# Kernel optimization log

Hardware: AMD Instinct MI355X
Metric: run time of the kernel (lower is better)

The kernel has to match this reference:

```python
import jax, jax.numpy as jnp
import numpy as np

EMBED_DIM = 1024
NUM_HEADS = 16
D_K = EMBED_DIM // NUM_HEADS


def setup_inputs() -> dict:
    key = jax.random.key(0)
    kx, kq, kk, kv, ko = jax.random.split(key, 5)
    scale = 1.0 / np.sqrt(EMBED_DIM)
    x = jax.random.normal(kx, (4, 2048, EMBED_DIM), dtype=jnp.float32)
    # Linear(embed_dim, embed_dim, bias=False) weights, stored [out, in] like torch
    Wq = jax.random.uniform(kq, (EMBED_DIM, EMBED_DIM), jnp.float32, -scale, scale)
    Wk = jax.random.uniform(kk, (EMBED_DIM, EMBED_DIM), jnp.float32, -scale, scale)
    Wv = jax.random.uniform(kv, (EMBED_DIM, EMBED_DIM), jnp.float32, -scale, scale)
    Wo = jax.random.uniform(ko, (EMBED_DIM, EMBED_DIM), jnp.float32, -scale, scale)
    return {"x": x, "Wq": Wq, "Wk": Wk, "Wv": Wv, "Wo": Wo}


def reference(x, Wq, Wk, Wv, Wo):
    b, s, _ = x.shape
    # torch Linear: y = x @ W.T
    def proj(W):
        y = jnp.einsum('bse,fe->bsf', x, W)
        return y.reshape(b, s, NUM_HEADS, D_K).transpose(0, 2, 1, 3)  # [b,h,s,d]
    q, k, v = proj(Wq), proj(Wk), proj(Wv)
    scores = jnp.einsum('bhqd,bhkd->bhqk', q, k) / jnp.sqrt(jnp.float32(D_K))
    attn = jax.nn.softmax(scores, axis=-1)  # dropout is identity in eval
    out = jnp.einsum('bhqk,bhkd->bhqd', attn, v)
    out = out.transpose(0, 2, 1, 3).reshape(b, s, EMBED_DIM)
    return jnp.einsum('bsf,ef->bse', out, Wo)
```

## Files before the change

### kernel.cpp

```cpp
#include <hip/hip_runtime.h>
#include <hip/hip_bf16.h>

typedef unsigned short u16;
typedef unsigned int   u32;
typedef __attribute__((ext_vector_type(8))) __bf16 bf16x8;
typedef __attribute__((ext_vector_type(2))) __bf16 bf16x2;
typedef __attribute__((ext_vector_type(8))) u16    ushort8v;
typedef __attribute__((ext_vector_type(2))) float  f32x2;
typedef __attribute__((ext_vector_type(4))) float  floatx4;

#define EMBED 1024
#define SEQ   2048
#define BATCH 4
#define NH    16
#define DKH   64
#define BHN   (BATCH*NH)
#define ZSTRIDE ((size_t)BHN*SEQ*DKH)

__device__ __forceinline__ u16 f2bf(float f){
  union { float f; unsigned u; } v; v.f = f;
  unsigned r = (v.u + 0x7FFFu + ((v.u >> 16) & 1u)) >> 16;
  return (u16)r;
}
__device__ __forceinline__ u32 pk2(float a, float b){
  f32x2 v = {a, b};
  return __builtin_bit_cast(u32, __builtin_convertvector(v, bf16x2));
}

__device__ __forceinline__ bf16x8 ld_frag(const u16* p){
  return __builtin_bit_cast(bf16x8, *(const ushort8v*)p);
}

__device__ __forceinline__ floatx4 mfma16(bf16x8 a, bf16x8 b, floatx4 c){
  return __builtin_amdgcn_mfma_f32_16x16x32_bf16(a, b, c, 0, 0, 0);
}

__device__ __forceinline__ void gl_lds16(const u16* g, u16* l){
  __builtin_amdgcn_global_load_lds((const __attribute__((address_space(1))) void*)g,
                                   (__attribute__((address_space(3))) void*)l,
                                   16, 0, 0);
}

#define CFENCE asm volatile("" ::: "memory")

__global__ __launch_bounds__(256) void cvt_all(const float* __restrict__ x,
    const float* __restrict__ wq, const float* __restrict__ wk,
    const float* __restrict__ wv, const float* __restrict__ wo,
    u16* __restrict__ Xb, u16* __restrict__ Wqb, u16* __restrict__ Wkb,
    u16* __restrict__ Wvb, u16* __restrict__ Wob){
  int b = blockIdx.x;
  const float* src; u16* dst; int i;
  if (b < 8192){ src = x; dst = Xb; i = b*256 + threadIdx.x; }
  else {
    int k = (b - 8192) >> 10, r = (b - 8192) & 1023;
    src = (k==0) ? wq : (k==1) ? wk : (k==2) ? wv : wo;
    dst = (k==0) ? Wqb : (k==1) ? Wkb : (k==2) ? Wvb : Wob;
    i = r*256 + threadIdx.x;
  }
  float4 v = ((const float4*)src)[i];
  ushort4 o;
  o.x = f2bf(v.x); o.y = f2bf(v.y); o.z = f2bf(v.z); o.w = f2bf(v.w);
  ((ushort4*)dst)[i] = o;
}

#define QSCALE 0.1803368801111204f
__global__ __launch_bounds__(256, 2) void gemm_qkv(const u16* __restrict__ X,
    const u16* __restrict__ Wq, const u16* __restrict__ Wk, const u16* __restrict__ Wv,
    u16* __restrict__ QKV){
  __shared__ __attribute__((aligned(16))) u16 As[2*128*32];
  __shared__ __attribute__((aligned(16))) u16 Bs[3][2*128*32];

  const int tid = threadIdx.x, lane = tid & 63, w = tid >> 6;
  const int lm = lane & 15, quad = lane >> 4;
  const int wm = (w & 1) * 64, wn = (w >> 1) * 64;
  const int m0 = blockIdx.x * 128, n0 = blockIdx.y * 128;
  const int row0 = tid >> 2, kc = tid & 3;

  const u16* A0 = X  + (size_t)(m0 + row0)*EMBED + kc*8;
  const u16* B0[3] = {
    Wq + (size_t)(n0 + row0)*EMBED + kc*8,
    Wk + (size_t)(n0 + row0)*EMBED + kc*8,
    Wv + (size_t)(n0 + row0)*EMBED + kc*8 };

  floatx4 acc[3][4][4];
  #pragma unroll
  for (int z = 0; z < 3; ++z)
    #pragma unroll
    for (int mi = 0; mi < 4; ++mi)
      #pragma unroll
      for (int ni = 0; ni < 4; ++ni)
        acc[z][mi][ni] = (floatx4){0.f, 0.f, 0.f, 0.f};

  gl_lds16(A0,            As + tid*8);
  gl_lds16(A0 + 64*EMBED, As + (256 + tid)*8);
  #pragma unroll
  for (int z = 0; z < 3; ++z){
    gl_lds16(B0[z],            Bs[z] + tid*8);
    gl_lds16(B0[z] + 64*EMBED, Bs[z] + (256 + tid)*8);
  }

  for (int kt = 0; kt < EMBED/32; ++kt){
    const int cur = kt & 1;
    __builtin_amdgcn_s_barrier();
    CFENCE;
    if (kt + 1 < EMBED/32){
      const int k0 = (kt + 1) * 32;
      gl_lds16(A0 + k0,            As + (cur^1)*4096 + tid*8);
      gl_lds16(A0 + 64*EMBED + k0, As + (cur^1)*4096 + (256 + tid)*8);
      #pragma unroll
      for (int z = 0; z < 3; ++z){
        gl_lds16(B0[z] + k0,            Bs[z] + (cur^1)*4096 + tid*8);
        gl_lds16(B0[z] + 64*EMBED + k0, Bs[z] + (cur^1)*4096 + (256 + tid)*8);
      }
      asm volatile("s_waitcnt vmcnt(8)" ::: "memory");
    } else {
      asm volatile("s_waitcnt vmcnt(0)" ::: "memory");
    }
    __builtin_amdgcn_s_barrier();
    CFENCE;
    const u16* Ac = As + cur*4096;
    bf16x8 af[4];
    #pragma unroll
    for (int mi = 0; mi < 4; ++mi)
      af[mi] = ld_frag(&Ac[(wm + mi*16 + lm)*32 + quad*8]);
    #pragma unroll
    for (int z = 0; z < 3; ++z){
      const u16* Bc = Bs[z] + cur*4096;
      bf16x8 bfz[4];
      #pragma unroll
      for (int ni = 0; ni < 4; ++ni)
        bfz[ni] = ld_frag(&Bc[(wn + ni*16 + lm)*32 + quad*8]);
      #pragma unroll
      for (int mi = 0; mi < 4; ++mi)
        #pragma unroll
        for (int ni = 0; ni < 4; ++ni)
          acc[z][mi][ni] = mfma16(af[mi], bfz[ni], acc[z][mi][ni]);
    }
  }

  #pragma unroll
  for (int z = 0; z < 2; ++z){
    const float scale = (z == 0) ? QSCALE : 1.0f;
    u16* outz = QKV + (size_t)z * ZSTRIDE;
    #pragma unroll
    for (int mi = 0; mi < 4; ++mi)
      #pragma unroll
      for (int ni = 0; ni < 4; ++ni)
        #pragma unroll
        for (int r = 0; r < 4; ++r){
          int m = m0 + wm + mi*16 + quad*4 + r;
          int n = n0 + wn + ni*16 + lm;
          int b = m >> 11, s = m & 2047, h = n >> 6, d = n & 63;
          outz[(((size_t)(b*NH + h))*SEQ + s)*DKH + d] = f2bf(acc[z][mi][ni][r] * scale);
        }
  }
  {
    u16* outz = QKV + (size_t)2 * ZSTRIDE;
    #pragma unroll
    for (int mi = 0; mi < 4; ++mi)
      #pragma unroll
      for (int ni = 0; ni < 4; ++ni){
        int mbase = m0 + wm + mi*16 + quad*4;
        int n = n0 + wn + ni*16 + lm;
        int b = mbase >> 11, sb = mbase & 2047;
        int h = n >> 6, d = n & 63;
        u16* dst = outz + (((size_t)(b*NH + h))*DKH + d)*SEQ + sb;
        uint2 pv;
        pv.x = pk2(acc[2][mi][ni][0], acc[2][mi][ni][1]);
        pv.y = pk2(acc[2][mi][ni][2], acc[2][mi][ni][3]);
        *reinterpret_cast<uint2*>(dst) = pv;
      }
  }
}

__global__ __launch_bounds__(256) void gemm_out(const u16* __restrict__ A,
    const u16* __restrict__ W, float* __restrict__ C){
  __shared__ __attribute__((aligned(16))) u16 As[2*128*64];
  __shared__ __attribute__((aligned(16))) u16 Bs[2*128*64];
  const int tid = threadIdx.x, lane = tid & 63, w = tid >> 6;
  const int lm = lane & 15, quad = lane >> 4;
  const int wm = (w & 1) * 64, wn = (w >> 1) * 64;
  const int m0 = blockIdx.x * 128, n0 = blockIdx.y * 128;

  const int srow = tid >> 3;
  const int ssw  = ((tid & 7) ^ (srow & 7)) * 8;
  const u16* Ab = A + (size_t)(m0 + srow)*EMBED + ssw;
  const u16* Bb = W + (size_t)(n0 + srow)*EMBED + ssw;

  floatx4 acc[4][4];
  #pragma unroll
  for (int mi = 0; mi < 4; ++mi)
    #pragma unroll
    for (int ni = 0; ni < 4; ++ni)
      acc[mi][ni] = (floatx4){0.f, 0.f, 0.f, 0.f};

  #pragma unroll
  for (int j = 0; j < 4; ++j){
    gl_lds16(Ab + (size_t)j*32*EMBED, As + (j*256 + tid)*8);
    gl_lds16(Bb + (size_t)j*32*EMBED, Bs + (j*256 + tid)*8);
  }

  for (int kt = 0; kt < EMBED/64; ++kt){
    const int cur = kt & 1;
    __builtin_amdgcn_s_barrier();
    CFENCE;
    if (kt + 1 < EMBED/64){
      const int k0 = (kt + 1) * 64;
      #pragma unroll
      for (int j = 0; j < 4; ++j){
        gl_lds16(Ab + (size_t)j*32*EMBED + k0, As + (cur^1)*8192 + (j*256 + tid)*8);
        gl_lds16(Bb + (size_t)j*32*EMBED + k0, Bs + (cur^1)*8192 + (j*256 + tid)*8);
      }
      asm volatile("s_waitcnt vmcnt(8)" ::: "memory");
    } else {
      asm volatile("s_waitcnt vmcnt(0)" ::: "memory");
    }
    __builtin_amdgcn_s_barrier();
    CFENCE;
    const u16* Ac = As + cur*8192;
    const u16* Bc = Bs + cur*8192;
    #pragma unroll
    for (int kh = 0; kh < 2; ++kh){
      const int us = ((kh*4 + quad) ^ (lm & 7)) * 8;
      bf16x8 af[4], bf[4];
      #pragma unroll
      for (int mi = 0; mi < 4; ++mi)
        af[mi] = ld_frag(&Ac[(wm + mi*16 + lm)*64 + us]);
      #pragma unroll
      for (int ni = 0; ni < 4; ++ni)
        bf[ni] = ld_frag(&Bc[(wn + ni*16 + lm)*64 + us]);
      #pragma unroll
      for (int mi = 0; mi < 4; ++mi)
        #pragma unroll
        for (int ni = 0; ni < 4; ++ni)
          acc[mi][ni] = mfma16(af[mi], bf[ni], acc[mi][ni]);
    }
  }

  #pragma unroll
  for (int mi = 0; mi < 4; ++mi)
    #pragma unroll
    for (int ni = 0; ni < 4; ++ni)
      #pragma unroll
      for (int r = 0; r < 4; ++r){
        int m = m0 + wm + mi*16 + quad*4 + r;
        int n = n0 + wn + ni*16 + lm;
        C[(size_t)m*EMBED + n] = acc[mi][ni][r];
      }
}

#define KSS 520
__global__ __launch_bounds__(256, 2) void attn_kernel(const u16* __restrict__ QKV,
                                                      u16* __restrict__ Out){
  __shared__ __attribute__((aligned(16))) u16 Ks[2][8*KSS];
  __shared__ __attribute__((aligned(16))) u16 Vs[2][64*64];

  const int tid = threadIdx.x, lane = tid & 63, w = tid >> 6;
  const int lm = lane & 15, quad = lane >> 4;
  const int bh = blockIdx.x;
  const int q0 = blockIdx.y * 256;
  const u16* Qh = QKV + (size_t)bh * SEQ * DKH;
  const u16* Kh = QKV + ZSTRIDE + (size_t)bh * SEQ * DKH;
  const u16* Vh = QKV + 2*ZSTRIDE + (size_t)bh * DKH * SEQ;

  const int sK = tid & 63, cK = tid >> 6;
  const int dV = tid >> 3, gV = tid & 7;
  const size_t vsrc0 = (size_t)dV * SEQ + ((gV ^ (dV & 7)) * 8);
  const size_t vsrc1 = vsrc0 + (size_t)32 * SEQ;

  bf16x8 qf[4][2];
  #pragma unroll
  for (int qt = 0; qt < 4; ++qt)
    #pragma unroll
    for (int st = 0; st < 2; ++st)
      qf[qt][st] = ld_frag(Qh + (size_t)(q0 + w*64 + qt*16 + lm)*DKH + st*32 + quad*8);

  const uint4 ONESW = {0x3F803F80u, 0x3F803F80u, 0x3F803F80u, 0x3F803F80u};
  const bf16x8 ones8 = __builtin_bit_cast(bf16x8, ONESW);

  floatx4 o[4][4], lac[4];
  #pragma unroll
  for (int qt = 0; qt < 4; ++qt){
    lac[qt] = (floatx4){0.f, 0.f, 0.f, 0.f};
    #pragma unroll
    for (int dt = 0; dt < 4; ++dt) o[qt][dt] = (floatx4){0.f, 0.f, 0.f, 0.f};
  }

  gl_lds16(Kh + (size_t)sK*DKH + cK*8,     Ks[0] + cK*KSS + sK*8);
  gl_lds16(Kh + (size_t)sK*DKH + (cK+4)*8, Ks[0] + (cK+4)*KSS + sK*8);
  gl_lds16(Vh + vsrc0,                     Vs[0] + tid*8);
  gl_lds16(Vh + vsrc1,                     Vs[0] + 2048 + tid*8);

  for (int kt = 0; kt < SEQ/64; ++kt){
    const int cur = kt & 1;
    __builtin_amdgcn_s_barrier();
    CFENCE;
    if (kt + 1 < SEQ/64){
      const int nk0 = (kt + 1) * 64;
      gl_lds16(Kh + (size_t)(nk0 + sK)*DKH + cK*8,     Ks[cur^1] + cK*KSS + sK*8);
      gl_lds16(Kh + (size_t)(nk0 + sK)*DKH + (cK+4)*8, Ks[cur^1] + (cK+4)*KSS + sK*8);
      gl_lds16(Vh + vsrc0 + nk0,                       Vs[cur^1] + tid*8);
      gl_lds16(Vh + vsrc1 + nk0,                       Vs[cur^1] + 2048 + tid*8);
      asm volatile("s_waitcnt vmcnt(4)" ::: "memory");
    } else {
      asm volatile("s_waitcnt vmcnt(0)" ::: "memory");
    }
    __builtin_amdgcn_s_barrier();
    CFENCE;
    const u16* Kc = Ks[cur];
    const u16* Vc = Vs[cur];

    #pragma unroll
    for (int u = 0; u < 2; ++u){
      uint2 e[4][2];
      #pragma unroll
      for (int half = 0; half < 2; ++half){
        const int t = u*2 + half;
        bf16x8 kf0 = ld_frag(&Kc[quad*KSS     + (t*16 + lm)*8]);
        bf16x8 kf1 = ld_frag(&Kc[(quad+4)*KSS + (t*16 + lm)*8]);
        #pragma unroll
        for (int qt = 0; qt < 4; ++qt){
          floatx4 s = (floatx4){0.f,0.f,0.f,0.f};
          s = mfma16(kf0, qf[qt][0], s);
          s = mfma16(kf1, qf[qt][1], s);
          e[qt][half].x = pk2(__builtin_amdgcn_exp2f(s[0]), __builtin_amdgcn_exp2f(s[1]));
          e[qt][half].y = pk2(__builtin_amdgcn_exp2f(s[2]), __builtin_amdgcn_exp2f(s[3]));
        }
      }
      bf16x8 pf[4];
      #pragma unroll
      for (int qt = 0; qt < 4; ++qt){
        uint4 pp = {e[qt][0].x, e[qt][0].y, e[qt][1].x, e[qt][1].y};
        pf[qt] = __builtin_bit_cast(bf16x8, pp);
      }
      #pragma unroll
      for (int qt = 0; qt < 4; ++qt)
        lac[qt] = mfma16(pf[qt], ones8, lac[qt]);
      const int cg0 = (((u*4     + (quad >> 1)) ^ (lm & 7)) * 8) + (quad & 1) * 4;
      const int cg1 = (((u*4 + 2 + (quad >> 1)) ^ (lm & 7)) * 8) + (quad & 1) * 4;
      #pragma unroll
      for (int dt = 0; dt < 4; ++dt){
        uint2 vlo = *(const uint2*)(Vc + (dt*16 + lm)*64 + cg0);
        uint2 vhi = *(const uint2*)(Vc + (dt*16 + lm)*64 + cg1);
        uint4 vv = {vlo.x, vlo.y, vhi.x, vhi.y};
        bf16x8 vb = __builtin_bit_cast(bf16x8, vv);
        #pragma unroll
        for (int qt = 0; qt < 4; ++qt)
          o[qt][dt] = mfma16(pf[qt], vb, o[qt][dt]);
      }
    }
  }

  const int bI = bh >> 4, h = bh & 15;
  #pragma unroll
  for (int qt = 0; qt < 4; ++qt){
    floatx4 inv;
    #pragma unroll
    for (int r = 0; r < 4; ++r) inv[r] = __builtin_amdgcn_rcpf(lac[qt][r]);
    #pragma unroll
    for (int dt = 0; dt < 4; ++dt)
      #pragma unroll
      for (int r = 0; r < 4; ++r){
        int s = q0 + w*64 + qt*16 + quad*4 + r;
        Out[((size_t)(bI*SEQ + s))*EMBED + h*DKH + dt*16 + lm] = f2bf(o[qt][dt][r] * inv[r]);
      }
  }
}

extern "C" void kernel_launch(void* const* d_in, const int* in_sizes, int n_in,
                              void* d_out, int out_size, void* d_ws, size_t ws_size,
                              hipStream_t stream){
  const float* x  = (const float*)d_in[0];
  const float* Wq = (const float*)d_in[1];
  const float* Wk = (const float*)d_in[2];
  const float* Wv = (const float*)d_in[3];
  const float* Wo = (const float*)d_in[4];
  float* out = (float*)d_out;

  char* ws = (char*)d_ws;
  u16* Xb  = (u16*)ws;
  u16* Wqb = (u16*)(ws + (size_t)16777216);
  u16* Wkb = Wqb + 1048576;
  u16* Wvb = Wkb + 1048576;
  u16* Wob = Wvb + 1048576;
  u16* QKV = (u16*)(ws + (size_t)25165824);
  u16* At  = (u16*)(ws + (size_t)75497472);

  cvt_all<<<12288, 256, 0, stream>>>(x, Wq, Wk, Wv, Wo, Xb, Wqb, Wkb, Wvb, Wob);
  gemm_qkv<<<dim3(64, 8), 256, 0, stream>>>(Xb, Wqb, Wkb, Wvb, QKV);
  attn_kernel<<<dim3(64, 8), 256, 0, stream>>>(QKV, At);
  gemm_out<<<dim3(64, 8), 256, 0, stream>>>(At, Wob, out);
}
```

Baseline: 247.3 us.

## Triple-buffer K/V tiles in attention kernel with single barrier per iteration

Replaces the double-buffered K/V LDS pipeline with a three-stage ring that prefetches two tiles ahead. The loop now waits for the current tile, issues one barrier, then starts the load for tile kt+2. This removes one barrier per iteration and hides more global-load latency. In exchange, LDS use per block rises by half, which could limit occupancy.

```diff
diff --git a/kernel.cpp b/kernel.cpp
--- a/kernel.cpp
+++ b/kernel.cpp
@@ -250,10 +250,11 @@
 }
 
 #define KSS 520
+#define NT  (SEQ/64)
 __global__ __launch_bounds__(256, 2) void attn_kernel(const u16* __restrict__ QKV,
                                                       u16* __restrict__ Out){
-  __shared__ __attribute__((aligned(16))) u16 Ks[2][8*KSS];
-  __shared__ __attribute__((aligned(16))) u16 Vs[2][64*64];
+  __shared__ __attribute__((aligned(16))) u16 Ks[3][8*KSS];
+  __shared__ __attribute__((aligned(16))) u16 Vs[3][64*64];
 
   const int tid = threadIdx.x, lane = tid & 63, w = tid >> 6;
   const int lm = lane & 15, quad = lane >> 4;
@@ -286,27 +287,28 @@
     for (int dt = 0; dt < 4; ++dt) o[qt][dt] = (floatx4){0.f, 0.f, 0.f, 0.f};
   }
 
-  gl_lds16(Kh + (size_t)sK*DKH + cK*8,     Ks[0] + cK*KSS + sK*8);
-  gl_lds16(Kh + (size_t)sK*DKH + (cK+4)*8, Ks[0] + (cK+4)*KSS + sK*8);
-  gl_lds16(Vh + vsrc0,                     Vs[0] + tid*8);
-  gl_lds16(Vh + vsrc1,                     Vs[0] + 2048 + tid*8);
-
-  for (int kt = 0; kt < SEQ/64; ++kt){
-    const int cur = kt & 1;
-    __builtin_amdgcn_s_barrier();
-    CFENCE;
-    if (kt + 1 < SEQ/64){
-      const int nk0 = (kt + 1) * 64;
-      gl_lds16(Kh + (size_t)(nk0 + sK)*DKH + cK*8,     Ks[cur^1] + cK*KSS + sK*8);
-      gl_lds16(Kh + (size_t)(nk0 + sK)*DKH + (cK+4)*8, Ks[cur^1] + (cK+4)*KSS + sK*8);
-      gl_lds16(Vh + vsrc0 + nk0,                       Vs[cur^1] + tid*8);
-      gl_lds16(Vh + vsrc1 + nk0,                       Vs[cur^1] + 2048 + tid*8);
-      asm volatile("s_waitcnt vmcnt(4)" ::: "memory");
-    } else {
-      asm volatile("s_waitcnt vmcnt(0)" ::: "memory");
-    }
-    __builtin_amdgcn_s_barrier();
-    CFENCE;
+  #pragma unroll
+  for (int p = 0; p < 2; ++p){
+    const int nk0 = p * 64;
+    gl_lds16(Kh + (size_t)(nk0 + sK)*DKH + cK*8,     Ks[p] + cK*KSS + sK*8);
+    gl_lds16(Kh + (size_t)(nk0 + sK)*DKH + (cK+4)*8, Ks[p] + (cK+4)*KSS + sK*8);
+    gl_lds16(Vh + vsrc0 + nk0,                       Vs[p] + tid*8);
+    gl_lds16(Vh + vsrc1 + nk0,                       Vs[p] + 2048 + tid*8);
+  }
+
+  int cur = 0, wb = 2;
+  for (int kt = 0; kt < NT; ++kt){
+    if (kt + 1 < NT) asm volatile("s_waitcnt vmcnt(4)" ::: "memory");
+    else             asm volatile("s_waitcnt vmcnt(0)" ::: "memory");
+    __builtin_amdgcn_s_barrier();
+    CFENCE;
+    if (kt + 2 < NT){
+      const int nk0 = (kt + 2) * 64;
+      gl_lds16(Kh + (size_t)(nk0 + sK)*DKH + cK*8,     Ks[wb] + cK*KSS + sK*8);
+      gl_lds16(Kh + (size_t)(nk0 + sK)*DKH + (cK+4)*8, Ks[wb] + (cK+4)*KSS + sK*8);
+      gl_lds16(Vh + vsrc0 + nk0,                       Vs[wb] + tid*8);
+      gl_lds16(Vh + vsrc1 + nk0,                       Vs[wb] + 2048 + tid*8);
+    }
     const u16* Kc = Ks[cur];
     const u16* Vc = Vs[cur];
 
@@ -349,6 +351,8 @@
           o[qt][dt] = mfma16(pf[qt], vb, o[qt][dt]);
       }
     }
+    cur = (cur == 2) ? 0 : cur + 1;
+    wb  = (wb  == 2) ? 0 : wb  + 1;
   }
 
   const int bI = bh >> 4, h = bh & 15;
```

New measurement: 241.3 us. -2.4%, faster.
